# Kernel optimization log

Hardware: AMD Instinct MI355X
Metric: run time of the kernel (lower is better)

The kernel has to match this reference:

```python
import jax, jax.numpy as jnp
import numpy as np

VOCAB = 100000
EMB = 256
HID = 512
H2 = HID // 2
TAGS = 6
START = 3
STOP = 4
NEG = -10000.0
T = 4096


def setup_inputs() -> dict:
    key = jax.random.key(0)
    ks = jax.random.split(key, 16)
    s = 0.05
    trans = jax.random.normal(ks[12], (TAGS, TAGS), dtype=jnp.float32)
    trans = trans.at[START, :].set(NEG).at[:, STOP].set(NEG)
    return {
        "sentence": jax.random.randint(ks[0], (T,), 0, VOCAB, dtype=jnp.int32),
        "emb": jax.random.normal(ks[1], (VOCAB, EMB), dtype=jnp.float32) * s,
        "w_ih_f": jax.random.normal(ks[2], (4 * H2, EMB), dtype=jnp.float32) * s,
        "w_hh_f": jax.random.normal(ks[3], (4 * H2, H2), dtype=jnp.float32) * s,
        "b_ih_f": jax.random.normal(ks[4], (4 * H2,), dtype=jnp.float32) * s,
        "b_hh_f": jax.random.normal(ks[5], (4 * H2,), dtype=jnp.float32) * s,
        "w_ih_b": jax.random.normal(ks[6], (4 * H2, EMB), dtype=jnp.float32) * s,
        "w_hh_b": jax.random.normal(ks[7], (4 * H2, H2), dtype=jnp.float32) * s,
        "b_ih_b": jax.random.normal(ks[8], (4 * H2,), dtype=jnp.float32) * s,
        "b_hh_b": jax.random.normal(ks[9], (4 * H2,), dtype=jnp.float32) * s,
        "W_out": jax.random.normal(ks[10], (TAGS, HID), dtype=jnp.float32) * s,
        "b_out": jax.random.normal(ks[11], (TAGS,), dtype=jnp.float32) * s,
        "transitions": trans,
        "h0": jax.random.normal(ks[13], (2, H2), dtype=jnp.float32),
        "c0": jax.random.normal(ks[14], (2, H2), dtype=jnp.float32),
    }


def _lstm_dir(x, h0, c0, w_ih, w_hh, b_ih, b_hh, reverse):
    # x: (T, E); PyTorch LSTM gate order i, f, g, o
    def step(carry, xt):
        h, c = carry
        z = xt @ w_ih.T + b_ih + h @ w_hh.T + b_hh
        i, f, g, o = jnp.split(z, 4)
        i = jax.nn.sigmoid(i)
        f = jax.nn.sigmoid(f)
        g = jnp.tanh(g)
        o = jax.nn.sigmoid(o)
        c = f * c + i * g
        h = o * jnp.tanh(c)
        return (h, c), h

    _, hs = jax.lax.scan(step, (h0, c0), x, reverse=reverse)
    return hs  # (T, H2), time-aligned for both directions


def reference(sentence, emb, w_ih_f, w_hh_f, b_ih_f, b_hh_f,
              w_ih_b, w_hh_b, b_ih_b, b_hh_b, W_out, b_out,
              transitions, h0, c0):
    x = emb[sentence]  # (T, E)
    hf = _lstm_dir(x, h0[0], c0[0], w_ih_f, w_hh_f, b_ih_f, b_hh_f, False)
    hb = _lstm_dir(x, h0[1], c0[1], w_ih_b, w_hh_b, b_ih_b, b_hh_b, True)
    feats = jnp.concatenate([hf, hb], axis=-1) @ W_out.T + b_out  # (T, TAGS)

    init = jnp.full((TAGS,), NEG, dtype=feats.dtype).at[START].set(0.0)

    def vstep(fv, feat):
        tmp = transitions + fv[None, :]          # (to, from)
        bp = jnp.argmax(tmp, axis=1)             # best prev tag per next tag
        fv_new = tmp[jnp.arange(TAGS), bp] + feat
        return fv_new, bp

    fv, bptrs = jax.lax.scan(vstep, init, feats)  # bptrs: (T, TAGS)
    term = fv + transitions[STOP]
    best = jnp.argmax(term)
    score = term[best]

    def btstep(tag, bp):
        return bp[tag], tag

    _, path = jax.lax.scan(btstep, best, bptrs, reverse=True)  # (T,)
    return score, path
```

## Files before the change

### kernel.cpp

```cpp
#include <hip/hip_runtime.h>
#include <stdint.h>
#include <math.h>

#define T 4096
#define NTAGS 6
#define START_TAG 3
#define STOP_TAG 4
#define NEGV -10000.0f

__device__ __forceinline__ float sigm_fast(float z) {
  return 1.f / (1.f + __expf(-z));
}
__device__ __forceinline__ float tanh_fast(float z) {
  return 1.f - 2.f / (1.f + __expf(2.f * z));
}

typedef _Float16 half2v __attribute__((ext_vector_type(2)));
__device__ __forceinline__ float dot2acc(unsigned a, unsigned b, float c) {
  return __builtin_amdgcn_fdot2(__builtin_bit_cast(half2v, a),
                                __builtin_bit_cast(half2v, b), c, false);
}
__device__ __forceinline__ unsigned short f16b(float x) {
  _Float16 h = (_Float16)x;
  return __builtin_bit_cast(unsigned short, h);
}

__global__ __launch_bounds__(256) void k0_prep(
    const float* __restrict__ wf, const float* __restrict__ wb,
    const float* __restrict__ bif, const float* __restrict__ bhf,
    const float* __restrict__ bib, const float* __restrict__ bhb,
    float* __restrict__ wT, float* __restrict__ bias2) {
  int idx = blockIdx.x * 256 + threadIdx.x;
  int k = idx >> 11, col = idx & 2047;
  int d = col >> 10, g = col & 1023;
  const float* w = d ? wb : wf;
  wT[idx] = w[g * 256 + k];
  if (idx < 2048) bias2[idx] = d ? (bib[g] + bhb[g]) : (bif[g] + bhf[g]);
}

__global__ __launch_bounds__(256) void k1_zpre(
    const int* __restrict__ sent, const float* __restrict__ emb,
    const float* __restrict__ wT, const float* __restrict__ bias2,
    float* __restrict__ zpre) {
  int tb = blockIdx.x, cb = blockIdx.y;
  int tid = threadIdx.x;
  int col = cb * 256 + tid;
  int d = col >> 10, g = col & 1023;
  __shared__ float xs[32 * 256];
  int t0 = tb * 32;
  for (int r = 0; r < 32; r++) {
    int s = sent[t0 + r];
    xs[r * 256 + tid] = emb[(size_t)s * 256 + tid];
  }
  __syncthreads();
  float acc[32];
#pragma unroll
  for (int r = 0; r < 32; r++) acc[r] = 0.f;
  const float4* xs4 = (const float4*)xs;
  for (int kq = 0; kq < 64; kq++) {
    float w0 = wT[(4 * kq + 0) * 2048 + col];
    float w1 = wT[(4 * kq + 1) * 2048 + col];
    float w2 = wT[(4 * kq + 2) * 2048 + col];
    float w3 = wT[(4 * kq + 3) * 2048 + col];
#pragma unroll
    for (int r = 0; r < 32; r++) {
      float4 x4 = xs4[r * 64 + kq];
      acc[r] += w0 * x4.x + w1 * x4.y + w2 * x4.z + w3 * x4.w;
    }
  }
  float bb = bias2[col];
  for (int r = 0; r < 32; r++)
    zpre[((size_t)d * T + (t0 + r)) * 1024 + g] = acc[r] + bb;
}

__global__ __launch_bounds__(256) void k2_lstm(
    const float* __restrict__ zpre,
    const float* __restrict__ whf, const float* __restrict__ whb,
    const float* __restrict__ h0, const float* __restrict__ c0,
    float* h_all, unsigned long long* ring) {
  int w = blockIdx.x;
  int d = w >> 4, sub = w & 15;
  const float* w_hh = d ? whb : whf;
  int tid = threadIdx.x;

  __shared__ uint4 wl4[8 * 256];
  __shared__ __align__(16) unsigned hpk[128];
  __shared__ float z_lds[64];

  {
    unsigned short* wlh = (unsigned short*)wl4;
    for (int idx = tid; idx < 64 * 256; idx += 256) {
      int sr = idx >> 8, sk = idx & 255;
      int sgate = sr >> 4, scl = sr & 15;
      int grow = sgate * 256 + sub * 16 + scl;
      float wv = w_hh[(size_t)grow * 256 + sk];
      int sq = sk >> 6, rem = sk & 63, sm = rem >> 3, sj = rem & 7;
      wlh[((sm * 256) + (sr * 4 + sq)) * 8 + sj] = f16b(wv);
    }
  }

  float c = 0.f;
  if (tid < 16) c = c0[d * 256 + sub * 16 + tid];

  const float* zp_d = zpre + (size_t)d * T * 1024;
  float* h_d = h_all + (size_t)d * T * 256;
  unsigned long long* rg = ring + (size_t)d * 2 * 256;

  int r = tid >> 2, q = tid & 3;
  int gate = r >> 4, cl = r & 15;
  size_t zoff = (size_t)gate * 256 + sub * 16 + cl;

  int chunk = tid >> 4;
  bool is_poll = (chunk != sub);

  if (tid < 128) {
    unsigned pa = (unsigned)f16b(h0[d * 256 + 2 * tid]);
    unsigned pb = (unsigned)f16b(h0[d * 256 + 2 * tid + 1]);
    hpk[tid] = pa | (pb << 16);
  }

  float zv = 0.f;
  if (q == 0) zv = zp_d[(size_t)(d ? (T - 1) : 0) * 1024 + zoff];
  __syncthreads();

  unsigned short* hpk_h = (unsigned short*)hpk;
  const uint4* hq = (const uint4*)hpk;

  for (int s = 0; s < T; s++) {
    int t = d ? (T - 1 - s) : s;
    float zv_next = 0.f;
    if (q == 0 && s + 1 < T) {
      int tn = d ? (t - 1) : (t + 1);
      zv_next = zp_d[(size_t)tn * 1024 + zoff];
    }

    if (s > 0) {
      if (is_poll) {
        unsigned exp_tag = (unsigned)(s - 1);
        unsigned long long* addr = &rg[((s - 1) & 1) * 256 + tid];
        unsigned long long v;
        do {
          v = __hip_atomic_load(addr, __ATOMIC_RELAXED, __HIP_MEMORY_SCOPE_AGENT);
        } while ((unsigned)(v >> 32) != exp_tag);
        union { unsigned u; float f; } cv; cv.u = (unsigned)v;
        hpk_h[tid] = f16b(cv.f);
      }
      __syncthreads();
    }

    float acc = 0.f;
#pragma unroll
    for (int m = 0; m < 8; m++) {
      uint4 wv4 = wl4[m * 256 + tid];
      uint4 hv4 = hq[q * 8 + m];
      acc = dot2acc(wv4.x, hv4.x, acc);
      acc = dot2acc(wv4.y, hv4.y, acc);
      acc = dot2acc(wv4.z, hv4.z, acc);
      acc = dot2acc(wv4.w, hv4.w, acc);
    }
    acc += __shfl_xor(acc, 1);
    acc += __shfl_xor(acc, 2);
    if (q == 0) {
      float z = acc + zv;
      z_lds[r] = (gate == 2) ? tanh_fast(z) : sigm_fast(z);
    }
    __syncthreads();

    if (tid < 16) {
      float iA = z_lds[tid], fA = z_lds[16 + tid];
      float gA = z_lds[32 + tid], oA = z_lds[48 + tid];
      c = fA * c + iA * gA;
      float hv = oA * tanh_fast(c);
      union { float f; unsigned u; } cv; cv.f = hv;
      __hip_atomic_store(&rg[(s & 1) * 256 + sub * 16 + tid],
                         ((unsigned long long)(unsigned)s << 32) | cv.u,
                         __ATOMIC_RELAXED, __HIP_MEMORY_SCOPE_AGENT);
      hpk_h[sub * 16 + tid] = f16b(hv);
      h_d[(size_t)t * 256 + sub * 16 + tid] = hv;
    }
    zv = zv_next;
  }
}

__global__ __launch_bounds__(64) void k3_feats(
    const float* __restrict__ h_all, const float* __restrict__ Wout,
    const float* __restrict__ bout, float* __restrict__ feats) {
  int t = blockIdx.x;
  int j = threadIdx.x;
  const float* hf = h_all + (size_t)t * 256;
  const float* hb = h_all + (size_t)T * 256 + (size_t)t * 256;
  float s[6];
#pragma unroll
  for (int g = 0; g < 6; g++) s[g] = 0.f;
#pragma unroll
  for (int m = 0; m < 4; m++) {
    float a = hf[j + 64 * m];
#pragma unroll
    for (int g = 0; g < 6; g++) s[g] += a * Wout[g * 512 + j + 64 * m];
  }
#pragma unroll
  for (int m = 0; m < 4; m++) {
    float b = hb[j + 64 * m];
#pragma unroll
    for (int g = 0; g < 6; g++) s[g] += b * Wout[g * 512 + 256 + j + 64 * m];
  }
#pragma unroll
  for (int g = 0; g < 6; g++) {
#pragma unroll
    for (int off = 32; off >= 1; off >>= 1) s[g] += __shfl_xor(s[g], off);
  }
  if (j < 6) feats[(size_t)t * 6 + j] = s[j] + bout[j];
}

__global__ __launch_bounds__(64) void k4_viterbi(
    const float* __restrict__ feats, const float* __restrict__ trans,
    float* __restrict__ out) {
  __shared__ unsigned char bp_lds[T * 8];
  __shared__ float fbuf[2][64 * 6];
  int lane = threadIdx.x;

  float tr[6];
#pragma unroll
  for (int f = 0; f < 6; f++) tr[f] = (lane < 6) ? trans[lane * 6 + f] : 0.f;
  float fv = (lane == START_TAG) ? 0.f : NEGV;

  for (int idx = lane; idx < 384; idx += 64) fbuf[0][idx] = feats[idx];

  for (int cch = 0; cch < 64; cch++) {
    float pf[6];
    if (cch + 1 < 64) {
#pragma unroll
      for (int m = 0; m < 6; m++)
        pf[m] = feats[(cch + 1) * 384 + lane + 64 * m];
    }
    const float* fb = fbuf[cch & 1];
    for (int j = 0; j < 64; j++) {
      int t = cch * 64 + j;
      float best = -3.4e38f;
      int bi = 0;
#pragma unroll
      for (int f = 0; f < 6; f++) {
        float v = __shfl(fv, f) + tr[f];
        if (v > best) { best = v; bi = f; }
      }
      float nfv = best + fb[j * 6 + (lane < 6 ? lane : 0)];
      if (lane < 6) {
        fv = nfv;
        bp_lds[t * 8 + lane] = (unsigned char)bi;
      }
    }
    if (cch + 1 < 64) {
#pragma unroll
      for (int m = 0; m < 6; m++)
        fbuf[(cch + 1) & 1][lane + 64 * m] = pf[m];
    }
  }

  float term = (lane < 6) ? (fv + trans[STOP_TAG * 6 + lane]) : -3.4e38f;
  float bestv = -3.4e38f;
  int bestt = 0;
#pragma unroll
  for (int f = 0; f < 6; f++) {
    float v = __shfl(term, f);
    if (v > bestv) { bestv = v; bestt = f; }
  }
  if (lane == 0) out[0] = bestv;

  unsigned int ident = 0;
#pragma unroll
  for (int i = 0; i < 6; i++) ident |= (unsigned)i << (3 * i);

  unsigned int p = ident;
  int base = lane * 64;
  for (int j2 = 0; j2 < 64; j2++) {
    const unsigned int* bw = (const unsigned int*)&bp_lds[(base + j2) * 8];
    unsigned int lo = bw[0], hi = bw[1];
    unsigned int mw = (lo & 7) | (((lo >> 8) & 7) << 3) | (((lo >> 16) & 7) << 6)
                    | (((lo >> 24) & 7) << 9) | ((hi & 7) << 12)
                    | (((hi >> 8) & 7) << 15);
    unsigned int np = 0;
#pragma unroll
    for (int i = 0; i < 6; i++) {
      unsigned int b = (mw >> (3 * i)) & 7;
      np |= ((p >> (3 * b)) & 7) << (3 * i);
    }
    p = np;
  }
  unsigned int suf = p;
#pragma unroll
  for (int off = 1; off < 64; off <<= 1) {
    unsigned int other = __shfl_down(suf, off);
    if (lane + off < 64) {
      unsigned int ns = 0;
#pragma unroll
      for (int i = 0; i < 6; i++) {
        unsigned int b = (other >> (3 * i)) & 7;
        ns |= ((suf >> (3 * b)) & 7) << (3 * i);
      }
      suf = ns;
    }
  }
  unsigned int tail = __shfl_down(suf, 1);
  if (lane == 63) tail = ident;
  unsigned int cur = tail;
  for (int j2 = 63; j2 >= 0; j2--) {
    int t = base + j2;
    out[1 + t] = (float)((cur >> (3 * bestt)) & 7);
    const unsigned int* bw = (const unsigned int*)&bp_lds[t * 8];
    unsigned int lo = bw[0], hi = bw[1];
    unsigned int mw = (lo & 7) | (((lo >> 8) & 7) << 3) | (((lo >> 16) & 7) << 6)
                    | (((lo >> 24) & 7) << 9) | ((hi & 7) << 12)
                    | (((hi >> 8) & 7) << 15);
    unsigned int nc = 0;
#pragma unroll
    for (int i = 0; i < 6; i++) {
      unsigned int b = (cur >> (3 * i)) & 7;
      nc |= ((mw >> (3 * b)) & 7) << (3 * i);
    }
    cur = nc;
  }
}

extern "C" void kernel_launch(void* const* d_in, const int* in_sizes, int n_in,
                              void* d_out, int out_size, void* d_ws, size_t ws_size,
                              hipStream_t stream) {
  const int*   sent  = (const int*)d_in[0];
  const float* emb   = (const float*)d_in[1];
  const float* wihf  = (const float*)d_in[2];
  const float* whhf  = (const float*)d_in[3];
  const float* bihf  = (const float*)d_in[4];
  const float* bhhf  = (const float*)d_in[5];
  const float* wihb  = (const float*)d_in[6];
  const float* whhb  = (const float*)d_in[7];
  const float* bihb  = (const float*)d_in[8];
  const float* bhhb  = (const float*)d_in[9];
  const float* Wout  = (const float*)d_in[10];
  const float* bout  = (const float*)d_in[11];
  const float* trans = (const float*)d_in[12];
  const float* h0    = (const float*)d_in[13];
  const float* c0    = (const float*)d_in[14];
  float* out = (float*)d_out;

  char* ws = (char*)d_ws;
  float*              zpre  = (float*)(ws + 0);
  float*              h_all = (float*)(ws + 33554432);
  float*              wT    = (float*)(ws + 41943040);
  float*              bias2 = (float*)(ws + 44040192);
  float*              feats = (float*)(ws + 44048384);
  unsigned long long* ring  = (unsigned long long*)(ws + 44146688);

  k0_prep<<<2048, 256, 0, stream>>>(wihf, wihb, bihf, bhhf, bihb, bhhb, wT, bias2);
  dim3 g1(128, 8);
  k1_zpre<<<g1, 256, 0, stream>>>(sent, emb, wT, bias2, zpre);
  k2_lstm<<<32, 256, 0, stream>>>(zpre, whhf, whhb, h0, c0, h_all, ring);
  k3_feats<<<4096, 64, 0, stream>>>(h_all, Wout, bout, feats);
  k4_viterbi<<<1, 64, 0, stream>>>(feats, trans, out);
}
```

Baseline: 6.717 ms.

## Split LSTM recurrence by K-quarter per wave and exchange packed fp16 hidden pairs

Restructures the per-step recurrent matvec so each of the four waves handles one quarter of the hidden dimension for all 64 gate rows. Each wave polls only the 32 ring entries it needs and syncs with a wave barrier instead of a block barrier, so the shuffle reductions go away and partial sums are combined through LDS. Each ring slot now carries two fp16 hidden values, which halves the ring size and the polling traffic. The step tag is shifted to s+1, and a second block barrier per step is added at the end of the loop.

```diff
diff --git a/kernel.cpp b/kernel.cpp
--- a/kernel.cpp
+++ b/kernel.cpp
@@ -82,103 +82,101 @@
   int d = w >> 4, sub = w & 15;
   const float* w_hh = d ? whb : whf;
   int tid = threadIdx.x;
-
-  __shared__ uint4 wl4[8 * 256];
-  __shared__ __align__(16) unsigned hpk[128];
-  __shared__ float z_lds[64];
+  int q = tid >> 6, lane = tid & 63;
+
+  __shared__ uint4 wl4[32 * 64];
+  __shared__ __align__(16) unsigned hq[4][32];
+  __shared__ float z_part[4][64];
 
   {
     unsigned short* wlh = (unsigned short*)wl4;
     for (int idx = tid; idx < 64 * 256; idx += 256) {
-      int sr = idx >> 8, sk = idx & 255;
-      int sgate = sr >> 4, scl = sr & 15;
-      int grow = sgate * 256 + sub * 16 + scl;
-      float wv = w_hh[(size_t)grow * 256 + sk];
-      int sq = sk >> 6, rem = sk & 63, sm = rem >> 3, sj = rem & 7;
-      wlh[((sm * 256) + (sr * 4 + sq)) * 8 + sj] = f16b(wv);
-    }
-  }
-
+      int r = idx >> 8, k = idx & 255;
+      int gate = r >> 4, cell = r & 15;
+      float wv = w_hh[(size_t)(gate * 256 + sub * 16 + cell) * 256 + k];
+      int sq = k >> 6, sm = (k >> 3) & 7, sj = k & 7;
+      wlh[((sq * 8 + sm) * 64 + r) * 8 + sj] = f16b(wv);
+    }
+  }
+  if (lane < 32) {
+    float f0 = h0[d * 256 + q * 64 + 2 * lane];
+    float f1 = h0[d * 256 + q * 64 + 2 * lane + 1];
+    hq[q][lane] = (unsigned)f16b(f0) | ((unsigned)f16b(f1) << 16);
+  }
   float c = 0.f;
   if (tid < 16) c = c0[d * 256 + sub * 16 + tid];
 
   const float* zp_d = zpre + (size_t)d * T * 1024;
   float* h_d = h_all + (size_t)d * T * 256;
-  unsigned long long* rg = ring + (size_t)d * 2 * 256;
-
-  int r = tid >> 2, q = tid & 3;
-  int gate = r >> 4, cl = r & 15;
-  size_t zoff = (size_t)gate * 256 + sub * 16 + cl;
-
-  int chunk = tid >> 4;
-  bool is_poll = (chunk != sub);
-
-  if (tid < 128) {
-    unsigned pa = (unsigned)f16b(h0[d * 256 + 2 * tid]);
-    unsigned pb = (unsigned)f16b(h0[d * 256 + 2 * tid + 1]);
-    hpk[tid] = pa | (pb << 16);
-  }
-
-  float zv = 0.f;
-  if (q == 0) zv = zp_d[(size_t)(d ? (T - 1) : 0) * 1024 + zoff];
+  unsigned long long* rg = ring + (size_t)d * 2 * 128;
+
+  float zv4[4] = {0.f, 0.f, 0.f, 0.f};
+  if (tid < 16) {
+    int t0 = d ? (T - 1) : 0;
+#pragma unroll
+    for (int g = 0; g < 4; g++)
+      zv4[g] = zp_d[(size_t)t0 * 1024 + g * 256 + sub * 16 + tid];
+  }
   __syncthreads();
-
-  unsigned short* hpk_h = (unsigned short*)hpk;
-  const uint4* hq = (const uint4*)hpk;
 
   for (int s = 0; s < T; s++) {
     int t = d ? (T - 1 - s) : s;
-    float zv_next = 0.f;
-    if (q == 0 && s + 1 < T) {
+    float zn4[4] = {0.f, 0.f, 0.f, 0.f};
+    if (tid < 16 && s + 1 < T) {
       int tn = d ? (t - 1) : (t + 1);
-      zv_next = zp_d[(size_t)tn * 1024 + zoff];
-    }
-
-    if (s > 0) {
-      if (is_poll) {
-        unsigned exp_tag = (unsigned)(s - 1);
-        unsigned long long* addr = &rg[((s - 1) & 1) * 256 + tid];
-        unsigned long long v;
-        do {
-          v = __hip_atomic_load(addr, __ATOMIC_RELAXED, __HIP_MEMORY_SCOPE_AGENT);
-        } while ((unsigned)(v >> 32) != exp_tag);
-        union { unsigned u; float f; } cv; cv.u = (unsigned)v;
-        hpk_h[tid] = f16b(cv.f);
-      }
-      __syncthreads();
-    }
-
+#pragma unroll
+      for (int g = 0; g < 4; g++)
+        zn4[g] = zp_d[(size_t)tn * 1024 + g * 256 + sub * 16 + tid];
+    }
+
+    if (s > 0 && lane < 32) {
+      unsigned exp_tag = (unsigned)s;
+      unsigned long long* addr = &rg[((s - 1) & 1) * 128 + q * 32 + lane];
+      unsigned long long v;
+      do {
+        v = __hip_atomic_load(addr, __ATOMIC_RELAXED, __HIP_MEMORY_SCOPE_AGENT);
+      } while ((unsigned)(v >> 32) != exp_tag);
+      hq[q][lane] = (unsigned)v;
+    }
+    __builtin_amdgcn_wave_barrier();
+
+    const uint4* hv = (const uint4*)hq[q];
     float acc = 0.f;
 #pragma unroll
     for (int m = 0; m < 8; m++) {
-      uint4 wv4 = wl4[m * 256 + tid];
-      uint4 hv4 = hq[q * 8 + m];
+      uint4 wv4 = wl4[(q * 8 + m) * 64 + lane];
+      uint4 hv4 = hv[m];
       acc = dot2acc(wv4.x, hv4.x, acc);
       acc = dot2acc(wv4.y, hv4.y, acc);
       acc = dot2acc(wv4.z, hv4.z, acc);
       acc = dot2acc(wv4.w, hv4.w, acc);
     }
-    acc += __shfl_xor(acc, 1);
-    acc += __shfl_xor(acc, 2);
-    if (q == 0) {
-      float z = acc + zv;
-      z_lds[r] = (gate == 2) ? tanh_fast(z) : sigm_fast(z);
-    }
+    z_part[q][lane] = acc;
     __syncthreads();
 
     if (tid < 16) {
-      float iA = z_lds[tid], fA = z_lds[16 + tid];
-      float gA = z_lds[32 + tid], oA = z_lds[48 + tid];
-      c = fA * c + iA * gA;
-      float hv = oA * tanh_fast(c);
-      union { float f; unsigned u; } cv; cv.f = hv;
-      __hip_atomic_store(&rg[(s & 1) * 256 + sub * 16 + tid],
-                         ((unsigned long long)(unsigned)s << 32) | cv.u,
-                         __ATOMIC_RELAXED, __HIP_MEMORY_SCOPE_AGENT);
-      hpk_h[sub * 16 + tid] = f16b(hv);
-      h_d[(size_t)t * 256 + sub * 16 + tid] = hv;
-    }
-    zv = zv_next;
+      float a[4];
+#pragma unroll
+      for (int g = 0; g < 4; g++) {
+        int r = g * 16 + tid;
+        float z = z_part[0][r] + z_part[1][r] + z_part[2][r] + z_part[3][r]
+                + zv4[g];
+        a[g] = (g == 2) ? tanh_fast(z) : sigm_fast(z);
+      }
+      c = a[1] * c + a[0] * a[2];
+      float hvl = a[3] * tanh_fast(c);
+      h_d[(size_t)t * 256 + sub * 16 + tid] = hvl;
+      float hn = __shfl_down(hvl, 1);
+      if ((tid & 1) == 0) {
+        unsigned h2 = (unsigned)f16b(hvl) | ((unsigned)f16b(hn) << 16);
+        __hip_atomic_store(&rg[(s & 1) * 128 + sub * 8 + (tid >> 1)],
+                           ((unsigned long long)(unsigned)(s + 1) << 32) | h2,
+                           __ATOMIC_RELAXED, __HIP_MEMORY_SCOPE_AGENT);
+      }
+#pragma unroll
+      for (int g = 0; g < 4; g++) zv4[g] = zn4[g];
+    }
+    __syncthreads();
   }
 }
 
```

After: 6.478 ms. -3.6%, faster.
